# Performance work log

Hardware: AMD Instinct MI355X
Metric: run time of the kernel (lower is better)

The kernel has to match this reference:

```python
import jax, jax.numpy as jnp
import numpy as np

B, N, D, H = 4, 1024, 1024, 16
DH = D // H  # 64
FF = 4 * D   # 4096


def _layernorm(x, w, b, eps=1e-5):
    mu = jnp.mean(x, axis=-1, keepdims=True)
    var = jnp.var(x, axis=-1, keepdims=True)
    return (x - mu) * jax.lax.rsqrt(var + eps) * w + b


def setup_inputs() -> dict:
    key = jax.random.key(0)
    ks = jax.random.split(key, 8)
    s = 0.02
    return {
        "x": jax.random.normal(ks[0], (B, N, D), jnp.float32),
        "ln1_w": jnp.ones((D,), jnp.float32),
        "ln1_b": jnp.zeros((D,), jnp.float32),
        "qkv_w": jax.random.normal(ks[1], (3 * D, D), jnp.float32) * s,
        "qkv_b": jnp.zeros((3 * D,), jnp.float32),
        "proj_l_w": jax.random.normal(ks[2], (H, H), jnp.float32) * s,
        "proj_l_b": jnp.zeros((H,), jnp.float32),
        "proj_w_w": jax.random.normal(ks[3], (H, H), jnp.float32) * s,
        "proj_w_b": jnp.zeros((H,), jnp.float32),
        "out_w": jax.random.normal(ks[4], (D, D), jnp.float32) * s,
        "out_b": jnp.zeros((D,), jnp.float32),
        "gamma1": jnp.ones((D,), jnp.float32),
        "ln2_w": jnp.ones((D,), jnp.float32),
        "ln2_b": jnp.zeros((D,), jnp.float32),
        "fc1_w": jax.random.normal(ks[5], (FF, D), jnp.float32) * s,
        "fc1_b": jnp.zeros((FF,), jnp.float32),
        "fc2_w": jax.random.normal(ks[6], (D, FF), jnp.float32) * s,
        "fc2_b": jnp.zeros((D,), jnp.float32),
        "gamma2": jnp.ones((D,), jnp.float32),
    }


def reference(x, ln1_w, ln1_b, qkv_w, qkv_b, proj_l_w, proj_l_b, proj_w_w,
              proj_w_b, out_w, out_b, gamma1, ln2_w, ln2_b, fc1_w, fc1_b,
              fc2_w, fc2_b, gamma2):
    # ---- LayerScale(TalkingHeadAttention) branch ----
    h = _layernorm(x, ln1_w, ln1_b)
    qkv = h @ qkv_w.T + qkv_b                      # [B,N,3D]
    q, k, v = jnp.split(qkv, 3, axis=-1)
    # [B,N,D] -> [B,H,N,DH]
    reshape = lambda t: t.reshape(B, N, H, DH).transpose(0, 2, 1, 3)
    q, k, v = reshape(q), reshape(k), reshape(v)
    attn = jnp.einsum("bhid,bhjd->bhij", q, k) * (DH ** -0.5)
    # talking-heads mixing before softmax (Linear over head dim)
    attn = jnp.einsum("bhij,gh->bgij", attn, proj_l_w) + proj_l_b[None, :, None, None]
    attn = jax.nn.softmax(attn, axis=-1)
    # talking-heads mixing after softmax
    attn = jnp.einsum("bhij,gh->bgij", attn, proj_w_w) + proj_w_b[None, :, None, None]
    o = jnp.einsum("bhij,bhjd->bhid", attn, v)     # [B,H,N,DH]
    o = o.transpose(0, 2, 1, 3).reshape(B, N, D)
    o = o @ out_w.T + out_b
    x = x + gamma1 * o
    # ---- LayerScale(MLP) branch ----
    h = _layernorm(x, ln2_w, ln2_b)
    h = jax.nn.gelu(h @ fc1_w.T + fc1_b)
    h = h @ fc2_w.T + fc2_b
    return x + gamma2 * h
```

## Files before the change

kernel.cpp:

```cpp
#include <hip/hip_runtime.h>


typedef _Float16 f16x8 __attribute__((ext_vector_type(8)));
typedef _Float16 f16x4 __attribute__((ext_vector_type(4)));
typedef _Float16 f16x2 __attribute__((ext_vector_type(2)));
typedef float f32x4 __attribute__((ext_vector_type(4)));

#define B_ 4
#define N_ 1024
#define D_ 1024
#define H_ 16
#define DH_ 64
#define FF_ 4096
#define M_ (B_ * N_)

__device__ __forceinline__ float gelu_act(float x) {
  float z = 0.7978845608028654f * (x + 0.044715f * x * x * x);
  return x / (1.0f + __expf(-2.0f * z));
}

__device__ __forceinline__ void ld_lds16(const _Float16* g, _Float16* l) {
  __builtin_amdgcn_global_load_lds((const __attribute__((address_space(1))) void*)g,
                                   (__attribute__((address_space(3))) void*)l, 16, 0, 0);
}

__device__ __forceinline__ int swz8(int i) {
  return (((i >> 2) << 1) ^ (i & 3)) & 7;
}
__device__ __forceinline__ int lds_off(int p, int i, int j) {
  int ch = ((j >> 3) ^ swz8(i) ^ ((p >> 2) << 1)) & 7;
  return p * 1032 + i * 64 + (ch << 3) + (j & 7);
}

__global__ __launch_bounds__(256) void cast_all(
    const float* __restrict__ a0, _Float16* __restrict__ o0,
    const float* __restrict__ a1, _Float16* __restrict__ o1,
    const float* __restrict__ a2, _Float16* __restrict__ o2,
    const float* __restrict__ a3, _Float16* __restrict__ o3,
    const float* __restrict__ W1, const float* __restrict__ W2,
    _Float16* __restrict__ w1f, _Float16* __restrict__ w2f,
    float* __restrict__ bsum) {
  int b = blockIdx.x, t = threadIdx.x;
  const float* in;
  _Float16* out;
  int base;
  if (b < 3072) { in = a0; out = o0; base = b; }
  else if (b < 4096) { in = a1; out = o1; base = b - 3072; }
  else if (b < 8192) { in = a2; out = o2; base = b - 4096; }
  else if (b < 12288) { in = a3; out = o3; base = b - 8192; }
  else {
    w1f[t] = (_Float16)W1[t];
    w2f[t] = (_Float16)W2[t];
    float4 z = {0.f, 0.f, 0.f, 0.f};
    #pragma unroll
    for (int r = 0; r < 4; r++) *(float4*)(bsum + t * 16 + r * 4) = z;
    return;
  }
  int i = (base * 256 + t) * 4;
  float4 v = *(const float4*)(in + i);
  f16x4 o;
  o[0] = (_Float16)v.x; o[1] = (_Float16)v.y; o[2] = (_Float16)v.z; o[3] = (_Float16)v.w;
  *(f16x4*)(out + i) = o;
}

__global__ __launch_bounds__(256) void ln_f16(const float* __restrict__ x,
                                              const float* __restrict__ w,
                                              const float* __restrict__ b,
                                              _Float16* __restrict__ out) {
  int row = blockIdx.x;
  int tid = threadIdx.x;
  const float* xr = x + (size_t)row * D_;
  float4 v = *(const float4*)(xr + tid * 4);
  float s = v.x + v.y + v.z + v.w;
  float sq = v.x * v.x + v.y * v.y + v.z * v.z + v.w * v.w;
  #pragma unroll
  for (int off = 32; off > 0; off >>= 1) {
    s += __shfl_down(s, off);
    sq += __shfl_down(sq, off);
  }
  __shared__ float red[8];
  int wave = tid >> 6, lane = tid & 63;
  if (lane == 0) { red[wave] = s; red[4 + wave] = sq; }
  __syncthreads();
  float ts = red[0] + red[1] + red[2] + red[3];
  float tq = red[4] + red[5] + red[6] + red[7];
  float mean = ts * (1.0f / (float)D_);
  float var = tq * (1.0f / (float)D_) - mean * mean;
  float rs = rsqrtf(var + 1e-5f);
  float4 wv = *(const float4*)(w + tid * 4);
  float4 bv = *(const float4*)(b + tid * 4);
  f16x4 o;
  o[0] = (_Float16)((v.x - mean) * rs * wv.x + bv.x);
  o[1] = (_Float16)((v.y - mean) * rs * wv.y + bv.y);
  o[2] = (_Float16)((v.z - mean) * rs * wv.z + bv.z);
  o[3] = (_Float16)((v.w - mean) * rs * wv.w + bv.w);
  *(f16x4*)(out + (size_t)row * D_ + tid * 4) = o;
}

template <int EPI, int BN, int OCC>
__global__ __launch_bounds__(256, OCC) void gemm_nt(
    const _Float16* __restrict__ A, const _Float16* __restrict__ W,
    const float* __restrict__ bias, int M, int N, int K,
    _Float16* __restrict__ outB, float* __restrict__ outF,
    const float* __restrict__ res, const float* __restrict__ gamma) {
  __shared__ _Float16 As[128 * 64];
  __shared__ _Float16 Bs[BN * 64];
  int tid = threadIdx.x;
  int wave = tid >> 6, lane = tid & 63;
  int quad = lane >> 4, l16 = lane & 15;
  int wm = wave >> 1, wn = wave & 1;
  int m0 = blockIdx.y * 128, n0 = blockIdx.x * BN;
  int lrow = lane >> 3, lcol = (lane & 7) * 8;
  const int NI = (BN == 128) ? 4 : 2;
  const int WN = (BN == 128) ? 64 : 32;

  f32x4 zero = {0.f, 0.f, 0.f, 0.f};
  f32x4 acc[4][NI];
  #pragma unroll
  for (int i = 0; i < 4; i++)
    #pragma unroll
    for (int j = 0; j < NI; j++) acc[i][j] = zero;

  for (int k0 = 0; k0 < K; k0 += 64) {
    __syncthreads();
    #pragma unroll
    for (int c = 0; c < 4; c++) {
      int rb = c * 32 + wave * 8;
      ld_lds16(A + (size_t)(m0 + rb + lrow) * K + k0 + lcol, As + rb * 64);
      if (BN == 128 || c < 2)
        ld_lds16(W + (size_t)(n0 + rb + lrow) * K + k0 + lcol, Bs + rb * 64);
    }
    __syncthreads();
    #pragma unroll
    for (int ks = 0; ks < 2; ks++) {
      int kk = ks * 32 + quad * 8;
      f16x8 a[4], bfr[NI];
      #pragma unroll
      for (int i = 0; i < 4; i++) a[i] = *(const f16x8*)(As + (wm * 64 + i * 16 + l16) * 64 + kk);
      #pragma unroll
      for (int i = 0; i < NI; i++) bfr[i] = *(const f16x8*)(Bs + (wn * WN + i * 16 + l16) * 64 + kk);
      #pragma unroll
      for (int mi = 0; mi < 4; mi++)
        #pragma unroll
        for (int ni = 0; ni < NI; ni++)
          acc[mi][ni] = __builtin_amdgcn_mfma_f32_16x16x32_f16(a[mi], bfr[ni], acc[mi][ni], 0, 0, 0);
    }
  }

  #pragma unroll
  for (int mi = 0; mi < 4; mi++) {
    int grow_base = m0 + wm * 64 + mi * 16 + quad * 4;
    #pragma unroll
    for (int ni = 0; ni < NI; ni++) {
      int gcol = n0 + wn * WN + ni * 16 + l16;
      float bb = bias[gcol];
      float gm = (EPI == 1) ? gamma[gcol] : 0.f;
      #pragma unroll
      for (int r = 0; r < 4; r++) {
        size_t oi = (size_t)(grow_base + r) * N + gcol;
        float c = acc[mi][ni][r] + bb;
        if (EPI == 0) {
          outB[oi] = (_Float16)c;
        } else if (EPI == 1) {
          outF[oi] = res[oi] + gm * c;
        } else {
          outB[oi] = (_Float16)gelu_act(c);
        }
      }
    }
  }
}

#define GPH_OPEN()                                      \
  __builtin_amdgcn_sched_barrier(0);                    \
  __builtin_amdgcn_s_barrier();                         \
  asm volatile("s_waitcnt lgkmcnt(0)" ::: "memory");    \
  __builtin_amdgcn_sched_barrier(0);                    \
  __builtin_amdgcn_s_setprio(1)

#define GPH_CLOSE()                                     \
  __builtin_amdgcn_s_setprio(0);                        \
  __builtin_amdgcn_sched_barrier(0);                    \
  __builtin_amdgcn_s_barrier()

#define GPH_CLOSE_VM(n)                                 \
  __builtin_amdgcn_s_setprio(0);                        \
  __builtin_amdgcn_sched_barrier(0);                    \
  asm volatile("s_waitcnt vmcnt(" #n ")" ::: "memory"); \
  __builtin_amdgcn_s_barrier()

#define GMFMA(MB, NB)                                                         \
  _Pragma("unroll") for (int ks = 0; ks < 2; ks++)                            \
  _Pragma("unroll") for (int mi = 0; mi < 4; mi++)                            \
  _Pragma("unroll") for (int ni = 0; ni < 2; ni++)                            \
    acc[MB + mi][NB + ni] = __builtin_amdgcn_mfma_f32_16x16x32_f16(           \
        ar[mi][ks], br[NB + ni][ks], acc[MB + mi][NB + ni], 0, 0, 0)

#define LDA(buf, MB)                                            \
  _Pragma("unroll") for (int ks = 0; ks < 2; ks++)              \
  _Pragma("unroll") for (int mi = 0; mi < 4; mi++)              \
    ar[mi][ks] = rdf(&lds[buf][0][wm][0], MB + mi, ks)

#define LDB(buf, NB)                                            \
  _Pragma("unroll") for (int ks = 0; ks < 2; ks++)              \
  _Pragma("unroll") for (int ni = 0; ni < 2; ni++)              \
    br[NB + ni][ks] = rdf(&lds[buf][1][wn >> 1][0], fbB + NB + ni, ks)

template <int EPI>
__global__ __launch_bounds__(512, 2) void gemm_nt8(
    const _Float16* __restrict__ A, const _Float16* __restrict__ W,
    const float* __restrict__ bias, int M, int N, int K,
    _Float16* __restrict__ outB) {
  __shared__ _Float16 lds[2][2][2][8192];
  const int tid = threadIdx.x;
  const int wv = tid >> 6, lane = tid & 63;
  const int quad = lane >> 4, l16 = lane & 15;
  const int wm = wv >> 2, wn = wv & 3;
  const int fbB = (wn & 1) * 4;
  const int wg = ((int)blockIdx.x & 7) * ((int)gridDim.x >> 3) + ((int)blockIdx.x >> 3);
  const int m0 = (wg & 15) << 8;
  const int n0 = (wg >> 4) << 8;
  const int gc = ((lane & 7) ^ (lane >> 3)) << 3;
  const int srow = wv * 8 + (lane >> 3);

  auto stageA = [&](int kt, int h) {
    const _Float16* g = A + (size_t)(m0 + h * 128 + srow) * K + kt * 64 + gc;
    _Float16* l = &lds[kt & 1][0][h][wv * 512];
    ld_lds16(g, l);
    ld_lds16(g + (size_t)64 * K, l + 4096);
  };
  auto stageB = [&](int kt, int h) {
    const _Float16* g = W + (size_t)(n0 + h * 128 + srow) * K + kt * 64 + gc;
    _Float16* l = &lds[kt & 1][1][h][wv * 512];
    ld_lds16(g, l);
    ld_lds16(g + (size_t)64 * K, l + 4096);
  };
  auto rdf = [&](const _Float16* base, int fi, int ks) -> f16x8 {
    int row = fi * 16 + l16;
    int pc = ((ks << 2) + quad) ^ (l16 & 7);
    return *(const f16x8*)(base + row * 64 + (pc << 3));
  };

  f32x4 acc[8][4];
  const f32x4 zero = {0.f, 0.f, 0.f, 0.f};
  #pragma unroll
  for (int i = 0; i < 8; i++)
    #pragma unroll
    for (int j = 0; j < 4; j++) acc[i][j] = zero;
  f16x8 ar[4][2], br[4][2];

  stageA(0, 0); stageA(0, 1); stageB(0, 0); stageB(0, 1);
  stageB(1, 0); stageB(1, 1);
  asm volatile("s_waitcnt vmcnt(4)" ::: "memory");
  __builtin_amdgcn_s_barrier();

  const int NT = K >> 6;
  const int ITERS = NT >> 1;
  for (int it = 0; it < ITERS - 1; ++it) {
    const int t0 = it * 2;
    LDA(0, 0); LDB(0, 0); stageA(t0 + 1, 0);
    GPH_OPEN(); GMFMA(0, 0); GPH_CLOSE();
    LDB(0, 2); stageA(t0 + 1, 1);
    GPH_OPEN(); GMFMA(0, 2); GPH_CLOSE();
    LDA(0, 4); stageB(t0 + 2, 0);
    GPH_OPEN(); GMFMA(4, 0); GPH_CLOSE();
    stageB(t0 + 2, 1);
    GPH_OPEN(); GMFMA(4, 2); GPH_CLOSE_VM(4);
    LDA(1, 0); LDB(1, 0); stageA(t0 + 2, 0);
    GPH_OPEN(); GMFMA(0, 0); GPH_CLOSE();
    LDB(1, 2); stageA(t0 + 2, 1);
    GPH_OPEN(); GMFMA(0, 2); GPH_CLOSE();
    LDA(1, 4); stageB(t0 + 3, 0);
    GPH_OPEN(); GMFMA(4, 0); GPH_CLOSE();
    stageB(t0 + 3, 1);
    GPH_OPEN(); GMFMA(4, 2); GPH_CLOSE_VM(4);
  }
  {
    LDA(0, 0); LDB(0, 0); stageA(NT - 1, 0);
    GPH_OPEN(); GMFMA(0, 0); GPH_CLOSE();
    LDB(0, 2); stageA(NT - 1, 1);
    GPH_OPEN(); GMFMA(0, 2); GPH_CLOSE();
    LDA(0, 4);
    GPH_OPEN(); GMFMA(4, 0); GPH_CLOSE();
    GPH_OPEN(); GMFMA(4, 2); GPH_CLOSE_VM(0);
    LDA(1, 0); LDB(1, 0);
    GPH_OPEN(); GMFMA(0, 0); GPH_CLOSE();
    LDB(1, 2);
    GPH_OPEN(); GMFMA(0, 2); GPH_CLOSE();
    LDA(1, 4);
    GPH_OPEN(); GMFMA(4, 0); GPH_CLOSE();
    GPH_OPEN(); GMFMA(4, 2); GPH_CLOSE();
  }

  #pragma unroll
  for (int mi = 0; mi < 8; mi++) {
    int grow = m0 + wm * 128 + mi * 16 + quad * 4;
    #pragma unroll
    for (int ni = 0; ni < 4; ni++) {
      int gcol = n0 + wn * 64 + ni * 16 + l16;
      float bb = bias[gcol];
      #pragma unroll
      for (int r = 0; r < 4; r++) {
        size_t oi = (size_t)(grow + r) * N + gcol;
        float c = acc[mi][ni][r] + bb;
        outB[oi] = (_Float16)(EPI == 2 ? gelu_act(c) : c);
      }
    }
  }
}

__global__ __launch_bounds__(256) void transpose_v(const _Float16* __restrict__ qkv,
                                                   _Float16* __restrict__ vt,
                                                   const float* __restrict__ b2,
                                                   float* __restrict__ bsum) {
  int jt = blockIdx.x;
  int h = blockIdx.y;
  int b = blockIdx.z;
  __shared__ _Float16 tl[64][68];
  int tid = threadIdx.x;
  int j0 = jt * 64;
  #pragma unroll
  for (int k = 0; k < 16; k++) {
    int idx = k * 256 + tid;
    int jr = idx >> 6, dc = idx & 63;
    tl[jr][dc] = qkv[(size_t)(b * N_ + j0 + jr) * (3 * D_) + 2 * D_ + h * 64 + dc];
  }
  __syncthreads();
  #pragma unroll
  for (int k = 0; k < 16; k++) {
    int idx = k * 256 + tid;
    int dr = idx >> 6, jc = idx & 63;
    vt[(size_t)((b * H_ + h) * DH_ + dr) * N_ + j0 + jc] = tl[jc][dr];
  }
  int d = tid & 63, jq = tid >> 6;
  float s = 0.f;
  #pragma unroll
  for (int r = 0; r < 16; r++) s += (float)tl[jq * 16 + r][d];
  atomicAdd(&bsum[b * D_ + h * 64 + d], b2[h] * s);
}

__global__ __launch_bounds__(1024, 4) void attn_th(
    const _Float16* __restrict__ qkv, const _Float16* __restrict__ vt,
    const _Float16* __restrict__ w1f, const _Float16* __restrict__ w2f,
    const float* __restrict__ b1f, const float* __restrict__ bsum,
    _Float16* __restrict__ ob) {
  __shared__ __align__(16) _Float16 SP[2 * 16512];
  __shared__ float lsum[272];
  _Float16* Sp = SP;
  _Float16* Pp = SP + 16512;

  const int tid = threadIdx.x;
  const int wave = tid >> 6;
  const int lane = tid & 63;
  const int quad = lane >> 4, l16 = lane & 15;
  const int i0 = blockIdx.x * 16;
  const int b = blockIdx.y;
  const size_t bN = (size_t)b * N_;
  const f32x4 zero = {0.f, 0.f, 0.f, 0.f};

  f16x8 qf[2];
  #pragma unroll
  for (int ks = 0; ks < 2; ks++) {
    f16x8 q = *(const f16x8*)(qkv + (bN + i0 + l16) * 3072 + wave * 64 + ks * 32 + quad * 8);
    #pragma unroll
    for (int e = 0; e < 8; e++) q[e] = q[e] * (_Float16)0.125f;
    qf[ks] = q;
  }
  f16x4 w1a = *(const f16x4*)(w1f + l16 * 16 + quad * 4);
  float b1v = b1f[l16];
  f32x4 b1i = {b1v, b1v, b1v, b1v};

  const _Float16* vbase = vt + (size_t)((b * H_ + wave) * DH_ + l16) * N_ + quad * 8;

  f32x4 uacc[4];
  #pragma unroll
  for (int nt = 0; nt < 4; nt++) uacc[nt] = zero;
  float lacc = 0.f;

  f16x8 kcur[4][2];
  auto loadK = [&](int j0) {
    #pragma unroll
    for (int jb = 0; jb < 4; jb++) {
      const _Float16* kb = qkv + (bN + j0 + jb * 16 + l16) * 3072 + 1024 + wave * 64 + quad * 8;
      kcur[jb][0] = *(const f16x8*)kb;
      kcur[jb][1] = *(const f16x8*)(kb + 32);
    }
  };
  loadK(0);

  f16x8 vreg[2][4];

  for (int t = 0; t < 16; t++) {
    int j0 = t * 64;
    #pragma unroll
    for (int h = 0; h < 2; h++)
      #pragma unroll
      for (int nt = 0; nt < 4; nt++)
        vreg[h][nt] = *(const f16x8*)(vbase + (size_t)(nt * 16) * N_ + j0 + h * 32);
    f32x4 sres[4];
    #pragma unroll
    for (int jb = 0; jb < 4; jb++) {
      f32x4 s = __builtin_amdgcn_mfma_f32_16x16x32_f16(kcur[jb][0], qf[0], zero, 0, 0, 0);
      sres[jb] = __builtin_amdgcn_mfma_f32_16x16x32_f16(kcur[jb][1], qf[1], s, 0, 0, 0);
    }
    #pragma unroll
    for (int jb = 0; jb < 4; jb++) {
      f16x4 sv;
      #pragma unroll
      for (int r = 0; r < 4; r++) sv[r] = (_Float16)sres[jb][r];
      *(f16x4*)(Sp + lds_off(wave, l16, jb * 16 + quad * 4)) = sv;
    }
    __syncthreads();
    if (t < 15) loadK(j0 + 64);
    #pragma unroll
    for (int cg = 0; cg < 4; cg++) {
      f16x4 sf;
      #pragma unroll
      for (int t4 = 0; t4 < 4; t4++)
        sf[t4] = Sp[lds_off(quad * 4 + t4, wave, cg * 16 + l16)];
      f32x4 a = __builtin_amdgcn_mfma_f32_16x16x16f16(sf, w1a, b1i, 0, 0, 0);
      f16x4 pv;
      #pragma unroll
      for (int r = 0; r < 4; r++) {
        float e = __expf(a[r]);
        lacc += e;
        pv[r] = (_Float16)e;
      }
      *(f16x4*)(Pp + lds_off(l16, wave, cg * 16 + quad * 4)) = pv;
    }
    __syncthreads();
    f16x8 pf0 = *(const f16x8*)(Pp + lds_off(wave, l16, quad * 8));
    f16x8 pf1 = *(const f16x8*)(Pp + lds_off(wave, l16, 32 + quad * 8));
    #pragma unroll
    for (int nt = 0; nt < 4; nt++)
      uacc[nt] = __builtin_amdgcn_mfma_f32_16x16x32_f16(vreg[0][nt], pf0, uacc[nt], 0, 0, 0);
    #pragma unroll
    for (int nt = 0; nt < 4; nt++)
      uacc[nt] = __builtin_amdgcn_mfma_f32_16x16x32_f16(vreg[1][nt], pf1, uacc[nt], 0, 0, 0);
  }

  lacc += __shfl_xor(lacc, 16);
  lacc += __shfl_xor(lacc, 32);
  __syncthreads();
  if (quad == 0) lsum[l16 * 17 + wave] = lacc;
  __syncthreads();
  float invl = 1.0f / lsum[wave * 17 + l16];

  _Float16* Uf = Sp;
  #pragma unroll
  for (int nt = 0; nt < 4; nt++) {
    f16x4 u;
    #pragma unroll
    for (int r = 0; r < 4; r++) u[r] = (_Float16)(uacc[nt][r] * invl);
    *(f16x4*)(Uf + wave * 1092 + l16 * 68 + nt * 16 + quad * 4) = u;
  }
  __syncthreads();

  f16x4 w2a = *(const f16x4*)(w2f + l16 * 16 + quad * 4);
  #pragma unroll
  for (int cg = 0; cg < 4; cg++) {
    f16x4 af;
    #pragma unroll
    for (int t4 = 0; t4 < 4; t4++)
      af[t4] = Uf[(quad * 4 + t4) * 1092 + wave * 68 + cg * 16 + l16];
    f32x4 o = __builtin_amdgcn_mfma_f32_16x16x16f16(af, w2a, zero, 0, 0, 0);
    f32x4 bs = *(const f32x4*)(bsum + b * D_ + l16 * 64 + cg * 16 + quad * 4);
    f16x4 ov;
    #pragma unroll
    for (int r = 0; r < 4; r++) ov[r] = (_Float16)(o[r] + bs[r]);
    *(f16x4*)(ob + (bN + i0 + wave) * D_ + l16 * 64 + cg * 16 + quad * 4) = ov;
  }
}

extern "C" void kernel_launch(void* const* d_in, const int* in_sizes, int n_in,
                              void* d_out, int out_size, void* d_ws, size_t ws_size,
                              hipStream_t stream) {
  const float* x      = (const float*)d_in[0];
  const float* ln1_w  = (const float*)d_in[1];
  const float* ln1_b  = (const float*)d_in[2];
  const float* qkv_w  = (const float*)d_in[3];
  const float* qkv_b  = (const float*)d_in[4];
  const float* plw    = (const float*)d_in[5];
  const float* plb    = (const float*)d_in[6];
  const float* pww    = (const float*)d_in[7];
  const float* pwb    = (const float*)d_in[8];
  const float* out_w  = (const float*)d_in[9];
  const float* out_b  = (const float*)d_in[10];
  const float* gamma1 = (const float*)d_in[11];
  const float* ln2_w  = (const float*)d_in[12];
  const float* ln2_b  = (const float*)d_in[13];
  const float* fc1_w  = (const float*)d_in[14];
  const float* fc1_b  = (const float*)d_in[15];
  const float* fc2_w  = (const float*)d_in[16];
  const float* fc2_b  = (const float*)d_in[17];
  const float* gamma2 = (const float*)d_in[18];
  float* out = (float*)d_out;

  char* ws = (char*)d_ws;
  _Float16* wq   = (_Float16*)(ws + 0);
  _Float16* wo   = (_Float16*)(ws + 6291456);
  _Float16* wf1  = (_Float16*)(ws + 8388608);
  _Float16* wf2  = (_Float16*)(ws + 16777216);
  float*    x1   = (float*)   (ws + 25165824);
  _Float16* ob   = (_Float16*)(ws + 41943040);
  _Float16* hb   = (_Float16*)(ws + 50331648);
  _Float16* qkvb = (_Float16*)(ws + 58720256);
  _Float16* vtb  = (_Float16*)(ws + 83886080);
  _Float16* fb   = (_Float16*)(ws + 58720256);
  _Float16* w1f  = (_Float16*)(ws + 25165824);
  _Float16* w2f  = (_Float16*)(ws + 25165824 + 512);
  float*    bsum = (float*)   (ws + 25165824 + 1024);
  if (ws_size < 92274688) return;

  cast_all<<<12289, 256, 0, stream>>>(qkv_w, wq, out_w, wo, fc1_w, wf1, fc2_w, wf2,
                                      plw, pww, w1f, w2f, bsum);

  ln_f16<<<4096, 256, 0, stream>>>(x, ln1_w, ln1_b, hb);
  gemm_nt8<0><<<192, 512, 0, stream>>>(hb, wq, qkv_b, M_, 3 * D_, D_, qkvb);
  transpose_v<<<dim3(16, 16, 4), 256, 0, stream>>>(qkvb, vtb, pwb, bsum);
  attn_th<<<dim3(64, 4), 1024, 0, stream>>>(qkvb, vtb, w1f, w2f, plb, bsum, ob);
  gemm_nt<1, 64, 4><<<dim3(16, 32), 256, 0, stream>>>(ob, wo, out_b, M_, D_, D_, nullptr, x1, x, gamma1);

  ln_f16<<<4096, 256, 0, stream>>>(x1, ln2_w, ln2_b, hb);
  gemm_nt8<2><<<256, 512, 0, stream>>>(hb, wf1, fc1_b, M_, FF_, D_, fb);
  gemm_nt<1, 64, 4><<<dim3(16, 32), 256, 0, stream>>>(fb, wf2, fc2_b, M_, D_, FF_, nullptr, out, x1, gamma2);
}
```

Baseline: 476.3 us.

## Split attention over key halves with separate combine kernel for more blocks

The talking-heads attention kernel now splits the key dimension into two halves, launching 512 blocks instead of 256. Each block writes unnormalized partial outputs and partial softmax sums to workspace, and a new combine kernel merges them, normalizes, and applies the post-softmax head mixing. The goal is better GPU occupancy and less register pressure, partly by streaming V loads instead of holding them all in registers. The fc2 weight cast moves to a separate launch after attention because its workspace slot is reused. This adds extra global traffic for the partial results and two more kernel launches.

```diff
diff --git a/kernel.cpp b/kernel.cpp
--- a/kernel.cpp
+++ b/kernel.cpp
@@ -32,11 +32,20 @@
   return p * 1032 + i * 64 + (ch << 3) + (j & 7);
 }
 
+__global__ __launch_bounds__(256) void cast_f32_f16(const float* __restrict__ in,
+                                                    _Float16* __restrict__ out, int n) {
+  int i = (blockIdx.x * 256 + threadIdx.x) * 4;
+  if (i >= n) return;
+  float4 v = *(const float4*)(in + i);
+  f16x4 o;
+  o[0] = (_Float16)v.x; o[1] = (_Float16)v.y; o[2] = (_Float16)v.z; o[3] = (_Float16)v.w;
+  *(f16x4*)(out + i) = o;
+}
+
 __global__ __launch_bounds__(256) void cast_all(
     const float* __restrict__ a0, _Float16* __restrict__ o0,
     const float* __restrict__ a1, _Float16* __restrict__ o1,
     const float* __restrict__ a2, _Float16* __restrict__ o2,
-    const float* __restrict__ a3, _Float16* __restrict__ o3,
     const float* __restrict__ W1, const float* __restrict__ W2,
     _Float16* __restrict__ w1f, _Float16* __restrict__ w2f,
     float* __restrict__ bsum) {
@@ -47,7 +56,6 @@
   if (b < 3072) { in = a0; out = o0; base = b; }
   else if (b < 4096) { in = a1; out = o1; base = b - 3072; }
   else if (b < 8192) { in = a2; out = o2; base = b - 4096; }
-  else if (b < 12288) { in = a3; out = o3; base = b - 8192; }
   else {
     w1f[t] = (_Float16)W1[t];
     w2f[t] = (_Float16)W2[t];
@@ -339,13 +347,11 @@
   atomicAdd(&bsum[b * D_ + h * 64 + d], b2[h] * s);
 }
 
-__global__ __launch_bounds__(1024, 4) void attn_th(
+__global__ __launch_bounds__(1024, 8) void attn_th(
     const _Float16* __restrict__ qkv, const _Float16* __restrict__ vt,
-    const _Float16* __restrict__ w1f, const _Float16* __restrict__ w2f,
-    const float* __restrict__ b1f, const float* __restrict__ bsum,
-    _Float16* __restrict__ ob) {
+    const _Float16* __restrict__ w1f, const float* __restrict__ b1f,
+    _Float16* __restrict__ Up, float* __restrict__ lp) {
   __shared__ __align__(16) _Float16 SP[2 * 16512];
-  __shared__ float lsum[272];
   _Float16* Sp = SP;
   _Float16* Pp = SP + 16512;
 
@@ -353,8 +359,10 @@
   const int wave = tid >> 6;
   const int lane = tid & 63;
   const int quad = lane >> 4, l16 = lane & 15;
-  const int i0 = blockIdx.x * 16;
-  const int b = blockIdx.y;
+  const int bid = blockIdx.x;
+  const int b = bid & 3;
+  const int s = (bid >> 2) & 1;
+  const int i0 = (bid >> 3) << 4;
   const size_t bN = (size_t)b * N_;
   const f32x4 zero = {0.f, 0.f, 0.f, 0.f};
 
@@ -386,22 +394,18 @@
       kcur[jb][1] = *(const f16x8*)(kb + 32);
     }
   };
-  loadK(0);
-
-  f16x8 vreg[2][4];
-
-  for (int t = 0; t < 16; t++) {
-    int j0 = t * 64;
-    #pragma unroll
-    for (int h = 0; h < 2; h++)
-      #pragma unroll
-      for (int nt = 0; nt < 4; nt++)
-        vreg[h][nt] = *(const f16x8*)(vbase + (size_t)(nt * 16) * N_ + j0 + h * 32);
+  const int sbase = s << 9;
+  loadK(sbase);
+
+  f16x8 vreg[4];
+
+  for (int t = 0; t < 8; t++) {
+    int j0 = sbase + t * 64;
     f32x4 sres[4];
     #pragma unroll
     for (int jb = 0; jb < 4; jb++) {
-      f32x4 s = __builtin_amdgcn_mfma_f32_16x16x32_f16(kcur[jb][0], qf[0], zero, 0, 0, 0);
-      sres[jb] = __builtin_amdgcn_mfma_f32_16x16x32_f16(kcur[jb][1], qf[1], s, 0, 0, 0);
+      f32x4 sr = __builtin_amdgcn_mfma_f32_16x16x32_f16(kcur[jb][0], qf[0], zero, 0, 0, 0);
+      sres[jb] = __builtin_amdgcn_mfma_f32_16x16x32_f16(kcur[jb][1], qf[1], sr, 0, 0, 0);
     }
     #pragma unroll
     for (int jb = 0; jb < 4; jb++) {
@@ -410,8 +414,11 @@
       for (int r = 0; r < 4; r++) sv[r] = (_Float16)sres[jb][r];
       *(f16x4*)(Sp + lds_off(wave, l16, jb * 16 + quad * 4)) = sv;
     }
+    if (t < 7) loadK(j0 + 64);
+    #pragma unroll
+    for (int nt = 0; nt < 4; nt++)
+      vreg[nt] = *(const f16x8*)(vbase + (size_t)(nt * 16) * N_ + j0);
     __syncthreads();
-    if (t < 15) loadK(j0 + 64);
     #pragma unroll
     for (int cg = 0; cg < 4; cg++) {
       f16x4 sf;
@@ -433,42 +440,74 @@
     f16x8 pf1 = *(const f16x8*)(Pp + lds_off(wave, l16, 32 + quad * 8));
     #pragma unroll
     for (int nt = 0; nt < 4; nt++)
-      uacc[nt] = __builtin_amdgcn_mfma_f32_16x16x32_f16(vreg[0][nt], pf0, uacc[nt], 0, 0, 0);
-    #pragma unroll
-    for (int nt = 0; nt < 4; nt++)
-      uacc[nt] = __builtin_amdgcn_mfma_f32_16x16x32_f16(vreg[1][nt], pf1, uacc[nt], 0, 0, 0);
+      uacc[nt] = __builtin_amdgcn_mfma_f32_16x16x32_f16(vreg[nt], pf0, uacc[nt], 0, 0, 0);
+    #pragma unroll
+    for (int nt = 0; nt < 4; nt++) {
+      f16x8 vf = *(const f16x8*)(vbase + (size_t)(nt * 16) * N_ + j0 + 32);
+      uacc[nt] = __builtin_amdgcn_mfma_f32_16x16x32_f16(vf, pf1, uacc[nt], 0, 0, 0);
+    }
   }
 
   lacc += __shfl_xor(lacc, 16);
   lacc += __shfl_xor(lacc, 32);
-  __syncthreads();
-  if (quad == 0) lsum[l16 * 17 + wave] = lacc;
-  __syncthreads();
-  float invl = 1.0f / lsum[wave * 17 + l16];
-
-  _Float16* Uf = Sp;
+  if (quad == 0) lp[(((size_t)s * B_ + b) * H_ + l16) * N_ + i0 + wave] = lacc;
+  const size_t ub = ((((size_t)s * B_ + b) * H_ + wave) * N_ + i0 + l16) * 64;
   #pragma unroll
   for (int nt = 0; nt < 4; nt++) {
     f16x4 u;
     #pragma unroll
-    for (int r = 0; r < 4; r++) u[r] = (_Float16)(uacc[nt][r] * invl);
-    *(f16x4*)(Uf + wave * 1092 + l16 * 68 + nt * 16 + quad * 4) = u;
+    for (int r = 0; r < 4; r++) u[r] = (_Float16)uacc[nt][r];
+    *(f16x4*)(Up + ub + nt * 16 + quad * 4) = u;
+  }
+}
+
+__global__ __launch_bounds__(256) void attn_combine(
+    const _Float16* __restrict__ Up, const float* __restrict__ lp,
+    const _Float16* __restrict__ w2f, const float* __restrict__ bsum,
+    _Float16* __restrict__ ob) {
+  const int i0 = blockIdx.x * 16;
+  const int b = blockIdx.y;
+  const int t = threadIdx.x;
+  __shared__ float w2s[256];
+  __shared__ float linv[16][17];
+  {
+    int e = t >> 4, il = t & 15;
+    float l0 = lp[((size_t)(0 * B_ + b) * H_ + e) * N_ + i0 + il];
+    float l1 = lp[((size_t)(1 * B_ + b) * H_ + e) * N_ + i0 + il];
+    linv[e][il] = 1.0f / (l0 + l1);
+    w2s[t] = (float)w2f[t];
   }
   __syncthreads();
-
-  f16x4 w2a = *(const f16x4*)(w2f + l16 * 16 + quad * 4);
-  #pragma unroll
-  for (int cg = 0; cg < 4; cg++) {
-    f16x4 af;
-    #pragma unroll
-    for (int t4 = 0; t4 < 4; t4++)
-      af[t4] = Uf[(quad * 4 + t4) * 1092 + wave * 68 + cg * 16 + l16];
-    f32x4 o = __builtin_amdgcn_mfma_f32_16x16x16f16(af, w2a, zero, 0, 0, 0);
-    f32x4 bs = *(const f32x4*)(bsum + b * D_ + l16 * 64 + cg * 16 + quad * 4);
+  const int il = t >> 4, dg = (t & 15) * 4;
+  const size_t s1off = (size_t)B_ * H_ * N_ * 64;
+  float o[16][4];
+  #pragma unroll
+  for (int g = 0; g < 16; g++)
+    #pragma unroll
+    for (int r = 0; r < 4; r++) o[g][r] = 0.f;
+  for (int e = 0; e < 16; e++) {
+    size_t ubr = (((size_t)b * H_ + e) * N_ + i0 + il) * 64 + dg;
+    f16x4 u0 = *(const f16x4*)(Up + ubr);
+    f16x4 u1 = *(const f16x4*)(Up + s1off + ubr);
+    float li = linv[e][il];
+    float un[4];
+    #pragma unroll
+    for (int r = 0; r < 4; r++) un[r] = ((float)u0[r] + (float)u1[r]) * li;
+    #pragma unroll
+    for (int g = 0; g < 16; g++) {
+      float w = w2s[g * 16 + e];
+      #pragma unroll
+      for (int r = 0; r < 4; r++) o[g][r] += w * un[r];
+    }
+  }
+  const size_t rowbase = ((size_t)b * N_ + i0 + il) * D_;
+  #pragma unroll
+  for (int g = 0; g < 16; g++) {
+    f32x4 bs = *(const f32x4*)(bsum + b * D_ + g * 64 + dg);
     f16x4 ov;
     #pragma unroll
-    for (int r = 0; r < 4; r++) ov[r] = (_Float16)(o[r] + bs[r]);
-    *(f16x4*)(ob + (bN + i0 + wave) * D_ + l16 * 64 + cg * 16 + quad * 4) = ov;
+    for (int r = 0; r < 4; r++) ov[r] = (_Float16)(o[g][r] + bs[r]);
+    *(f16x4*)(ob + rowbase + g * 64 + dg) = ov;
   }
 }
 
@@ -507,18 +546,22 @@
   _Float16* qkvb = (_Float16*)(ws + 58720256);
   _Float16* vtb  = (_Float16*)(ws + 83886080);
   _Float16* fb   = (_Float16*)(ws + 58720256);
-  _Float16* w1f  = (_Float16*)(ws + 25165824);
-  _Float16* w2f  = (_Float16*)(ws + 25165824 + 512);
-  float*    bsum = (float*)   (ws + 25165824 + 1024);
+  _Float16* w1f  = (_Float16*)(ws + 16777216);
+  _Float16* w2f  = (_Float16*)(ws + 16777216 + 512);
+  float*    bsum = (float*)   (ws + 16777216 + 1024);
+  float*    lp   = (float*)   (ws + 16777216 + 17408);
+  _Float16* Up   = (_Float16*)(ws + 25165824);
   if (ws_size < 92274688) return;
 
-  cast_all<<<12289, 256, 0, stream>>>(qkv_w, wq, out_w, wo, fc1_w, wf1, fc2_w, wf2,
-                                      plw, pww, w1f, w2f, bsum);
+  cast_all<<<8193, 256, 0, stream>>>(qkv_w, wq, out_w, wo, fc1_w, wf1,
+                                     plw, pww, w1f, w2f, bsum);
 
   ln_f16<<<4096, 256, 0, stream>>>(x, ln1_w, ln1_b, hb);
   gemm_nt8<0><<<192, 512, 0, stream>>>(hb, wq, qkv_b, M_, 3 * D_, D_, qkvb);
   transpose_v<<<dim3(16, 16, 4), 256, 0, stream>>>(qkvb, vtb, pwb, bsum);
-  attn_th<<<dim3(64, 4), 1024, 0, stream>>>(qkvb, vtb, w1f, w2f, plb, bsum, ob);
+  attn_th<<<512, 1024, 0, stream>>>(qkvb, vtb, w1f, plb, Up, lp);
+  attn_combine<<<dim3(64, 4), 256, 0, stream>>>(Up, lp, w2f, bsum, ob);
+  cast_f32_f16<<<4096, 256, 0, stream>>>(fc2_w, wf2, 4096 * 1024);
   gemm_nt<1, 64, 4><<<dim3(16, 32), 256, 0, stream>>>(ob, wo, out_b, M_, D_, D_, nullptr, x1, x, gamma1);
 
   ln_f16<<<4096, 256, 0, stream>>>(x1, ln2_w, ln2_b, hb);
```

Result: slower. 670.1 us (+40.7%).
